# Kernel optimization log

Hardware: AMD Instinct MI355X
Metric: run time of the kernel (lower is better)

The kernel has to match this reference:

```python
import jax, jax.numpy as jnp
import numpy as np

B, P, N, E, H, D = 8, 1000, 1000, 128, 8, 16  # batch, pomo, nodes, embed, heads, qkv_dim
SQRT_E = float(np.sqrt(E))
CLIP = 10.0
INV_SQRT_D = 1.0 / float(np.sqrt(D))


def _heads(x):
    # [b, n, H*D] -> [b, H, n, D]
    b, n, _ = x.shape
    return x.reshape(b, n, H, D).transpose(0, 2, 1, 3)


def _mha(q, k, v, ninf_mask):
    # q: [b,H,P,D], k/v: [b,H,N,D], ninf_mask: [b,P,N]
    score = jnp.einsum('bhnd,bhsd->bhns', q, k) * INV_SQRT_D
    score = score + ninf_mask[:, None, :, :]
    w = jax.nn.softmax(score, axis=-1)
    out = jnp.einsum('bhns,bhsd->bhnd', w, v)
    return out.transpose(0, 2, 1, 3).reshape(q.shape[0], q.shape[2], H * D)


def setup_inputs() -> dict:
    key = jax.random.key(0)
    ks = jax.random.split(key, 16)
    s = 0.02
    return {
        'encoded_last_node': jax.random.normal(ks[0], (B, P, E), jnp.float32),
        'attr': jax.random.normal(ks[1], (B, P, 4), jnp.float32),
        'encoded_nodes': jax.random.normal(ks[2], (B, N, E), jnp.float32),
        'ninf_mask': jnp.zeros((B, P, N), jnp.float32),
        'Wq_shared': jax.random.normal(ks[3], (E + 4, H * D), jnp.float32) * s,
        'Wk_shared': jax.random.normal(ks[4], (E, H * D), jnp.float32) * s,
        'Wv_shared': jax.random.normal(ks[5], (E, H * D), jnp.float32) * s,
        'Wq_task': jax.random.normal(ks[6], (E + 4, H * D), jnp.float32) * s,
        'Wk_task': jax.random.normal(ks[7], (E, H * D), jnp.float32) * s,
        'Wv_task': jax.random.normal(ks[8], (E, H * D), jnp.float32) * s,
        'Wc_shared': jax.random.normal(ks[9], (H * D, E), jnp.float32) * s,
        'bc_shared': jnp.zeros((E,), jnp.float32),
        'Wc_task': jax.random.normal(ks[10], (H * D, E), jnp.float32) * s,
        'bc_task': jnp.zeros((E,), jnp.float32),
        'Wg': jax.random.normal(ks[11], (E + 4, E), jnp.float32) * s,
        'bg': jnp.zeros((E,), jnp.float32),
    }


def reference(encoded_last_node, attr, encoded_nodes, ninf_mask,
              Wq_shared, Wk_shared, Wv_shared, Wq_task, Wk_task, Wv_task,
              Wc_shared, bc_shared, Wc_task, bc_task, Wg, bg):
    # set_kv
    k_shared = _heads(encoded_nodes @ Wk_shared)
    v_shared = _heads(encoded_nodes @ Wv_shared)
    k_task = _heads(encoded_nodes @ Wk_task)
    v_task = _heads(encoded_nodes @ Wv_task)

    # decoder forward
    input_cat = jnp.concatenate([encoded_last_node, attr], axis=2)  # [B,P,E+4]
    q_shared = _heads(input_cat @ Wq_shared)
    q_task = _heads(input_cat @ Wq_task)

    out_shared = _mha(q_shared, k_shared, v_shared, ninf_mask) @ Wc_shared + bc_shared
    out_task = _mha(q_task, k_task, v_task, ninf_mask) @ Wc_task + bc_task

    gate = jax.nn.sigmoid(input_cat @ Wg + bg)
    gated_out = gate * out_shared + (1.0 - gate) * out_task  # [B,P,E]

    # pointer scores against single-head key (encoded_nodes)
    score = jnp.einsum('bpe,bne->bpn', gated_out, encoded_nodes) / SQRT_E
    score_clipped = CLIP * jnp.tanh(score)
    probs = jax.nn.softmax(score_clipped + ninf_mask, axis=2)
    return probs
```

## Files before the change

kernel.cpp:

```cpp
#include <hip/hip_runtime.h>
#include <math.h>

#define BB 8
#define PP 1000
#define NN 1000
#define EE 128
#define HH 8
#define DD 16

#define INV_SQRT_E 0.08838834764831845f
#define INV_SQRT_D 0.25f

typedef short short8_t __attribute__((ext_vector_type(8)));
typedef float f32x4    __attribute__((ext_vector_type(4)));
typedef float f32x16   __attribute__((ext_vector_type(16)));
typedef __bf16 bf16x4  __attribute__((ext_vector_type(4)));
typedef __bf16 bf16x8  __attribute__((ext_vector_type(8)));

__device__ __forceinline__ float sigmoid_fast(float x) {
    return 1.f / (1.f + __expf(-x));
}
__device__ __forceinline__ float tanh_fast(float x) {
    x = fminf(fmaxf(x, -15.f), 15.f);
    float e = __expf(2.f * x);
    return (e - 1.f) / (e + 1.f);
}

__device__ __forceinline__ f32x4 mfma16(short8_t a, short8_t b, f32x4 c) {
    return __builtin_amdgcn_mfma_f32_16x16x32_bf16(a, b, c, 0, 0, 0);
}
__device__ __forceinline__ f32x16 mfma32(short8_t a, short8_t b, f32x16 c) {
    return __builtin_amdgcn_mfma_f32_32x32x16_bf16(a, b, c, 0, 0, 0);
}

__device__ __forceinline__ float sum16(float x) {
    int v;
    v = __builtin_amdgcn_update_dpp(0, __builtin_bit_cast(int, x), 0xB1, 0xF, 0xF, true);
    x += __builtin_bit_cast(float, v);
    v = __builtin_amdgcn_update_dpp(0, __builtin_bit_cast(int, x), 0x4E, 0xF, 0xF, true);
    x += __builtin_bit_cast(float, v);
    v = __builtin_amdgcn_update_dpp(0, __builtin_bit_cast(int, x), 0x141, 0xF, 0xF, true);
    x += __builtin_bit_cast(float, v);
    v = __builtin_amdgcn_update_dpp(0, __builtin_bit_cast(int, x), 0x140, 0xF, 0xF, true);
    x += __builtin_bit_cast(float, v);
    return x;
}

__device__ __forceinline__ unsigned int pack_bf16(float a, float b) {
    __bf16 x = (__bf16)a, y = (__bf16)b;
    unsigned short ux = __builtin_bit_cast(unsigned short, x);
    unsigned short uy = __builtin_bit_cast(unsigned short, y);
    return (unsigned int)ux | ((unsigned int)uy << 16);
}

__global__ __launch_bounds__(256) void conv_w_kernel(
    const float* __restrict__ Wk_s, const float* __restrict__ Wv_s,
    const float* __restrict__ Wk_t, const float* __restrict__ Wv_t,
    const float* __restrict__ Wq_s, const float* __restrict__ Wq_t,
    const float* __restrict__ Wg,   const float* __restrict__ Wc_s,
    const float* __restrict__ Wc_t, __bf16* __restrict__ Wtb)
{
    const int m = blockIdx.x, kt = blockIdx.y;
    const float* srcs[9] = {Wk_s, Wv_s, Wk_t, Wv_t, Wq_s, Wq_t, Wg, Wc_s, Wc_t};
    const int   srcKs[9] = {128, 128, 128, 128, 132, 132, 132, 128, 128};
    const int   kpads[9] = {128, 128, 128, 128, 160, 160, 160, 128, 128};
    const size_t offs[9] = {0, 16384, 32768, 49152, 65536, 86016, 106496, 126976, 143360};
    const int kp = kpads[m];
    if (kt * 32 >= kp) return;
    const float* src = srcs[m];
    const int sK = srcKs[m];
    const size_t off = offs[m];
    __shared__ float tile[32][129];
    const int tid = threadIdx.x;
    for (int j = tid; j < 32 * 128; j += 256) {
        int kk = j >> 7, n = j & 127;
        int k = kt * 32 + kk;
        tile[kk][n] = (k < sK) ? src[(size_t)k * 128 + n] : 0.f;
    }
    __syncthreads();
    for (int j = tid; j < 32 * 128; j += 256) {
        int n = j >> 5, kk = j & 31;
        Wtb[off + (size_t)n * kp + kt * 32 + kk] = (__bf16)tile[kk][n];
    }
}

__global__ __launch_bounds__(256) void to_bf16_kernel(
    const float* __restrict__ in, __bf16* __restrict__ outb)
{
    int i = (blockIdx.x * 256 + threadIdx.x) * 4;
    float4 v = *(const float4*)&in[i];
    bf16x4 pk = { (__bf16)v.x, (__bf16)v.y, (__bf16)v.z, (__bf16)v.w };
    *(bf16x4*)&outb[i] = pk;
}

__global__ __launch_bounds__(256) void concat_inb_kernel(
    const float* __restrict__ eln, const float* __restrict__ attr,
    __bf16* __restrict__ inb)
{
    int t = blockIdx.x * 256 + threadIdx.x;
    int row = t / 20, seg = t - row * 20;
    bf16x8 o = {};
    if (seg < 16) {
        const float* p = &eln[(size_t)row * 128 + seg * 8];
        float4 a = *(const float4*)p, b = *(const float4*)(p + 4);
        o = bf16x8{ (__bf16)a.x, (__bf16)a.y, (__bf16)a.z, (__bf16)a.w,
                    (__bf16)b.x, (__bf16)b.y, (__bf16)b.z, (__bf16)b.w };
    } else if (seg == 16) {
        float4 a = *(const float4*)&attr[(size_t)row * 4];
        o = bf16x8{ (__bf16)a.x, (__bf16)a.y, (__bf16)a.z, (__bf16)a.w,
                    (__bf16)0.f, (__bf16)0.f, (__bf16)0.f, (__bf16)0.f };
    }
    *(bf16x8*)&inb[(size_t)row * 160 + seg * 8] = o;
}

template<int NC>
__device__ __forceinline__ void proj_body(
    const __bf16* __restrict__ A, const __bf16* __restrict__ W,
    f32x4 acc[8], int r0, int quad, int lq)
{
    const int K = NC * 32;
    short8_t aF[NC];
    #pragma unroll
    for (int c = 0; c < NC; ++c)
        aF[c] = *(const short8_t*)&A[(size_t)(r0 + lq) * K + c * 32 + quad * 8];
    #pragma unroll
    for (int nt = 0; nt < 8; ++nt) {
        acc[nt] = f32x4{0.f, 0.f, 0.f, 0.f};
        #pragma unroll
        for (int c = 0; c < NC; ++c) {
            short8_t bF = *(const short8_t*)&W[(size_t)(nt * 16 + lq) * K + c * 32 + quad * 8];
            acc[nt] = mfma16(aF[c], bF, acc[nt]);
        }
    }
}

__global__ __launch_bounds__(256) void proj_mfma_kernel(
    const __bf16* __restrict__ nodesb, const __bf16* __restrict__ inb,
    const __bf16* __restrict__ Wtb, const float* __restrict__ bg,
    __bf16* __restrict__ kb_s, __bf16* __restrict__ vt_s,
    __bf16* __restrict__ kb_t, __bf16* __restrict__ vt_t,
    __bf16* __restrict__ qb_s, __bf16* __restrict__ qb_t,
    float* __restrict__ gate)
{
    const int wsel = blockIdx.y;
    const int wave = threadIdx.x >> 6, lane = threadIdx.x & 63;
    const int quad = lane >> 4, lq = lane & 15;
    const int r0 = blockIdx.x * 64 + wave * 16;

    f32x4 acc[8];
    if (wsel < 4) {
        proj_body<4>(nodesb, Wtb + (size_t)wsel * 16384, acc, r0, quad, lq);
    } else {
        proj_body<5>(inb, Wtb + 65536 + (size_t)(wsel - 4) * 20480, acc, r0, quad, lq);
    }

    if (wsel == 0 || wsel == 2 || wsel == 4 || wsel == 5) {
        __bf16* O = (wsel == 0) ? kb_s : (wsel == 2) ? kb_t : (wsel == 4) ? qb_s : qb_t;
        #pragma unroll
        for (int r = 0; r < 4; ++r) {
            int m = r0 + quad * 4 + r;
            int b = m / 1000, n = m - b * 1000;
            #pragma unroll
            for (int nt = 0; nt < 8; ++nt)
                O[(((size_t)(b * 8 + nt) * 1000 + n) << 4) + lq] = (__bf16)acc[nt][r];
        }
    } else if (wsel == 1 || wsel == 3) {
        __bf16* O = (wsel == 1) ? vt_s : vt_t;
        #pragma unroll
        for (int r = 0; r < 4; ++r) {
            int m = r0 + quad * 4 + r;
            int b = m / 1000, n = m - b * 1000;
            int rr = n & 31;
            int pos = (n & ~31) + ((rr < 16) ? (rr << 1) : (((rr - 16) << 1) | 1));
            #pragma unroll
            for (int nt = 0; nt < 8; ++nt)
                O[(((size_t)(b * 8 + nt) * 16 + lq) << 10) + pos] = (__bf16)acc[nt][r];
        }
    } else {
        #pragma unroll
        for (int nt = 0; nt < 8; ++nt) {
            float bias = bg[nt * 16 + lq];
            #pragma unroll
            for (int r = 0; r < 4; ++r) {
                int m = r0 + quad * 4 + r;
                gate[(size_t)m * 128 + nt * 16 + lq] = sigmoid_fast(acc[nt][r] + bias);
            }
        }
    }
}

__global__ __launch_bounds__(256) void attn_mfma_kernel(
    const __bf16* __restrict__ qb_s, const __bf16* __restrict__ qb_t,
    const __bf16* __restrict__ kb_s, const __bf16* __restrict__ kb_t,
    const __bf16* __restrict__ vt_s, const __bf16* __restrict__ vt_t,
    const float* __restrict__ mask,
    float* __restrict__ att_s, float* __restrict__ att_t)
{
    const int b    = blockIdx.z;
    const int wave = threadIdx.x >> 6;
    const int combo = blockIdx.y * 4 + wave;
    const int br = combo & 1;
    const int h  = combo >> 1;
    const __bf16* Q  = br ? qb_t : qb_s;
    const __bf16* K  = br ? kb_t : kb_s;
    const __bf16* Vt = br ? vt_t : vt_s;
    float* O         = br ? att_t : att_s;
    const int lane = threadIdx.x & 63;
    const int quad = lane >> 4, lq = lane & 15;
    const int col  = lane & 31;
    const int half = lane >> 5;
    const int bh = b * HH + h;
    const int p0 = blockIdx.x * 32;

    __shared__ __align__(16) __bf16 S[4][32][36];

    int pq = p0 + col; if (pq > 999) pq = 999;
    short8_t qA = *(const short8_t*)&Q[(((size_t)bh * 1000 + pq) << 4) + half * 8];

    short8_t onesB = { (short)0x3F80, (short)0x3F80, (short)0x3F80, (short)0x3F80,
                       (short)0x3F80, (short)0x3F80, (short)0x3F80, (short)0x3F80 };

    f32x4 o[2] = { {0.f,0.f,0.f,0.f}, {0.f,0.f,0.f,0.f} };
    f32x4 l[2] = { {0.f,0.f,0.f,0.f}, {0.f,0.f,0.f,0.f} };

    const float* mrow[8];
    #pragma unroll
    for (int j = 0; j < 8; ++j) {
        int row = p0 + ((2 * j) & 3) + 8 * (j >> 1) + 4 * half;
        if (row > 998) row = 998;
        mrow[j] = mask + ((size_t)b * 1000 + row) * 1000 + col;
    }

    short8_t kBc = *(const short8_t*)&K[(((size_t)bh * 1000 + col) << 4) + half * 8];
    short8_t vBc = *(const short8_t*)&Vt[(((size_t)bh * 16 + lq) << 10) + quad * 8];

    for (int n0 = 0; n0 < 992; n0 += 32) {
        int nk = n0 + 32 + col; if (nk > 999) nk = 999;
        short8_t kBn = *(const short8_t*)&K[(((size_t)bh * 1000 + nk) << 4) + half * 8];
        short8_t vBn = *(const short8_t*)&Vt[(((size_t)bh * 16 + lq) << 10) + n0 + 32 + quad * 8];

        float mk[16];
        #pragma unroll
        for (int j = 0; j < 8; ++j) {
            mk[2 * j]     = mrow[j][0];
            mk[2 * j + 1] = mrow[j][1000];
            mrow[j] += 32;
        }

        f32x16 s = mfma32(qA, kBc, f32x16{});

        __threadfence_block();
        #pragma unroll
        for (int reg = 0; reg < 16; ++reg) {
            float e = __expf(fmaf(s[reg], INV_SQRT_D, mk[reg]));
            S[wave][(reg & 3) + 8 * (reg >> 2) + 4 * half][col] = (__bf16)e;
        }
        __threadfence_block();

        #pragma unroll
        for (int t = 0; t < 2; ++t) {
            uint2 L = *(const uint2*)&S[wave][t * 16 + lq][quad * 4];
            uint2 H = *(const uint2*)&S[wave][t * 16 + lq][16 + quad * 4];
            unsigned u0 = __builtin_amdgcn_perm(H.x, L.x, 0x05040100u);
            unsigned u1 = __builtin_amdgcn_perm(H.x, L.x, 0x07060302u);
            unsigned u2 = __builtin_amdgcn_perm(H.y, L.y, 0x05040100u);
            unsigned u3 = __builtin_amdgcn_perm(H.y, L.y, 0x07060302u);
            uint4 u4 = make_uint4(u0, u1, u2, u3);
            short8_t aP = __builtin_bit_cast(short8_t, u4);
            o[t] = mfma16(aP, vBc, o[t]);
            l[t] = mfma16(aP, onesB, l[t]);
        }
        kBc = kBn; vBc = vBn;
    }

    {
        f32x16 s = mfma32(qA, kBc, f32x16{});
        __threadfence_block();
        #pragma unroll
        for (int reg = 0; reg < 16; ++reg) {
            int j = reg >> 1;
            float mkv = (col < 8) ? ((reg & 1) ? mrow[j][1000] : mrow[j][0]) : 0.f;
            float e = (col < 8) ? __expf(fmaf(s[reg], INV_SQRT_D, mkv)) : 0.f;
            S[wave][(reg & 3) + 8 * (reg >> 2) + 4 * half][col] = (__bf16)e;
        }
        __threadfence_block();
        #pragma unroll
        for (int t = 0; t < 2; ++t) {
            uint2 L = *(const uint2*)&S[wave][t * 16 + lq][quad * 4];
            uint2 H = *(const uint2*)&S[wave][t * 16 + lq][16 + quad * 4];
            unsigned u0 = __builtin_amdgcn_perm(H.x, L.x, 0x05040100u);
            unsigned u1 = __builtin_amdgcn_perm(H.x, L.x, 0x07060302u);
            unsigned u2 = __builtin_amdgcn_perm(H.y, L.y, 0x05040100u);
            unsigned u3 = __builtin_amdgcn_perm(H.y, L.y, 0x07060302u);
            uint4 u4 = make_uint4(u0, u1, u2, u3);
            short8_t aP = __builtin_bit_cast(short8_t, u4);
            o[t] = mfma16(aP, vBc, o[t]);
            l[t] = mfma16(aP, onesB, l[t]);
        }
    }

    #pragma unroll
    for (int t = 0; t < 2; ++t)
        #pragma unroll
        for (int r = 0; r < 4; ++r) {
            int p = p0 + t * 16 + quad * 4 + r;
            if (p < 1000)
                O[((size_t)b * 1000 + p) * 128 + h * 16 + lq] = o[t][r] / l[t][r];
        }
}

__global__ __launch_bounds__(256) void combine_mfma_kernel(
    const float* __restrict__ att_s, const float* __restrict__ att_t,
    const __bf16* __restrict__ Wtb,
    const float* __restrict__ bc_s, const float* __restrict__ bc_t,
    const float* __restrict__ gate, __bf16* __restrict__ gatedb)
{
    const int wave = threadIdx.x >> 6, lane = threadIdx.x & 63;
    const int quad = lane >> 4, lq = lane & 15;
    const int r0 = blockIdx.x * 64 + wave * 16;
    const __bf16* Ws = Wtb + 126976;
    const __bf16* Wt = Wtb + 143360;

    short8_t aS[4], aT[4];
    #pragma unroll
    for (int c = 0; c < 4; ++c) {
        const float* ps = &att_s[(size_t)(r0 + lq) * 128 + c * 32 + quad * 8];
        const float* pt = &att_t[(size_t)(r0 + lq) * 128 + c * 32 + quad * 8];
        float4 x = *(const float4*)ps, y = *(const float4*)(ps + 4);
        bf16x8 s8 = { (__bf16)x.x, (__bf16)x.y, (__bf16)x.z, (__bf16)x.w,
                      (__bf16)y.x, (__bf16)y.y, (__bf16)y.z, (__bf16)y.w };
        aS[c] = __builtin_bit_cast(short8_t, s8);
        x = *(const float4*)pt; y = *(const float4*)(pt + 4);
        bf16x8 t8 = { (__bf16)x.x, (__bf16)x.y, (__bf16)x.z, (__bf16)x.w,
                      (__bf16)y.x, (__bf16)y.y, (__bf16)y.z, (__bf16)y.w };
        aT[c] = __builtin_bit_cast(short8_t, t8);
    }
    f32x4 accS[8], accT[8];
    #pragma unroll
    for (int nt = 0; nt < 8; ++nt) {
        accS[nt] = f32x4{0.f,0.f,0.f,0.f};
        accT[nt] = f32x4{0.f,0.f,0.f,0.f};
        #pragma unroll
        for (int c = 0; c < 4; ++c) {
            short8_t bS = *(const short8_t*)&Ws[(size_t)(nt * 16 + lq) * 128 + c * 32 + quad * 8];
            short8_t bT = *(const short8_t*)&Wt[(size_t)(nt * 16 + lq) * 128 + c * 32 + quad * 8];
            accS[nt] = mfma16(aS[c], bS, accS[nt]);
            accT[nt] = mfma16(aT[c], bT, accT[nt]);
        }
    }
    #pragma unroll
    for (int nt = 0; nt < 8; ++nt) {
        int f = nt * 16 + lq;
        float b1 = bc_s[f], b2 = bc_t[f];
        #pragma unroll
        for (int r = 0; r < 4; ++r) {
            int m = r0 + quad * 4 + r;
            float g = gate[(size_t)m * 128 + f];
            float val = g * (accS[nt][r] + b1) + (1.f - g) * (accT[nt][r] + b2);
            gatedb[(size_t)m * 128 + f] = (__bf16)val;
        }
    }
}

__global__ __launch_bounds__(256) void pointer_softmax_kernel(
    const __bf16* __restrict__ gb, const __bf16* __restrict__ nb,
    const float* __restrict__ mask, float* __restrict__ out)
{
    const int b    = blockIdx.y;
    const int p0   = blockIdx.x * 16;
    const int wave = threadIdx.x >> 6;
    const int lane = threadIdx.x & 63;
    const int quad = lane >> 4, lq = lane & 15;

    __shared__ float Spart[4][16];

    short8_t aF[4];
    {
        int pp = p0 + lq; if (pp > 999) pp = 999;
        const __bf16* arow = gb + (((size_t)b * 1000 + pp) << 7) + quad * 8;
        #pragma unroll
        for (int kc = 0; kc < 4; ++kc) aF[kc] = *(const short8_t*)&arow[kc * 32];
    }

    float ev[16][4];
    float psum[4] = {0.f, 0.f, 0.f, 0.f};

    #pragma unroll
    for (int i = 0; i < 16; ++i) {
        const int nt = i * 4 + wave;
        const int nn = nt * 16 + lq;
        const bool nv = nn < 1000;
        int nc = nv ? nn : 999;
        const __bf16* brow = nb + (((size_t)b * 1000 + nc) << 7) + quad * 8;
        f32x4 acc = {0.f, 0.f, 0.f, 0.f};
        #pragma unroll
        for (int kc = 0; kc < 4; ++kc) {
            short8_t bF = *(const short8_t*)&brow[kc * 32];
            acc = mfma16(aF[kc], bF, acc);
        }
        #pragma unroll
        for (int r = 0; r < 4; ++r) {
            int p = p0 + quad * 4 + r;
            bool v = nv && (p < 1000);
            size_t midx = v ? ((size_t)b * 1000 + p) * 1000 + nn : 0;
            float mk = mask[midx];
            float sc = 10.f * tanh_fast(acc[r] * INV_SQRT_E);
            float ee = v ? __expf(sc + mk) : 0.f;
            ev[i][r] = ee;
            psum[r] += ee;
        }
    }

    #pragma unroll
    for (int r = 0; r < 4; ++r) psum[r] = sum16(psum[r]);
    if (lq == 0) {
        #pragma unroll
        for (int r = 0; r < 4; ++r) Spart[wave][quad * 4 + r] = psum[r];
    }
    __syncthreads();
    float inv[4];
    #pragma unroll
    for (int r = 0; r < 4; ++r) {
        int row = quad * 4 + r;
        float s = Spart[0][row] + Spart[1][row] + Spart[2][row] + Spart[3][row];
        inv[r] = 1.f / s;
    }

    #pragma unroll
    for (int i = 0; i < 16; ++i) {
        const int nt = i * 4 + wave;
        const int nn = nt * 16 + lq;
        if (nn < 1000) {
            #pragma unroll
            for (int r = 0; r < 4; ++r) {
                int p = p0 + quad * 4 + r;
                if (p < 1000)
                    out[((size_t)b * 1000 + p) * 1000 + nn] = ev[i][r] * inv[r];
            }
        }
    }
}

extern "C" void kernel_launch(void* const* d_in, const int* in_sizes, int n_in,
                              void* d_out, int out_size, void* d_ws, size_t ws_size,
                              hipStream_t stream)
{
    const float* eln   = (const float*)d_in[0];
    const float* attr  = (const float*)d_in[1];
    const float* nodes = (const float*)d_in[2];
    const float* mask  = (const float*)d_in[3];
    const float* Wq_s  = (const float*)d_in[4];
    const float* Wk_s  = (const float*)d_in[5];
    const float* Wv_s  = (const float*)d_in[6];
    const float* Wq_t  = (const float*)d_in[7];
    const float* Wk_t  = (const float*)d_in[8];
    const float* Wv_t  = (const float*)d_in[9];
    const float* Wc_s  = (const float*)d_in[10];
    const float* bc_s  = (const float*)d_in[11];
    const float* Wc_t  = (const float*)d_in[12];
    const float* bc_t  = (const float*)d_in[13];
    const float* Wg    = (const float*)d_in[14];
    const float* bg    = (const float*)d_in[15];
    float* out = (float*)d_out;

    char* w = (char*)d_ws;
    const size_t KB_SZ = (size_t)8 * 8 * 1000 * 16 * 2;
    const size_t VT_SZ = (size_t)8 * 8 * 16 * 1024 * 2;
    const size_t F_SZ  = (size_t)8000 * 128 * 4;
    const size_t H_SZ  = (size_t)8000 * 128 * 2;
    const size_t IN_SZ = (size_t)8000 * 160 * 2;
    __bf16* kb_s = (__bf16*)w;            w += KB_SZ;
    __bf16* kb_t = (__bf16*)w;            w += KB_SZ;
    __bf16* qb_s = (__bf16*)w;            w += KB_SZ;
    __bf16* qb_t = (__bf16*)w;            w += KB_SZ;
    __bf16* vt_s = (__bf16*)w;            w += VT_SZ;
    __bf16* vt_t = (__bf16*)w;            w += VT_SZ;
    float* gate  = (float*)w;             w += F_SZ;
    float* att_s = (float*)w;             w += F_SZ;
    float* att_t = (float*)w;             w += F_SZ;
    __bf16* gatedb = (__bf16*)w;          w += H_SZ;
    __bf16* nodesb = (__bf16*)w;          w += H_SZ;
    __bf16* inb    = (__bf16*)w;          w += IN_SZ;
    __bf16* Wtb    = (__bf16*)w;          w += 320000;

    hipMemsetAsync(vt_s, 0, 2 * VT_SZ, stream);

    conv_w_kernel<<<dim3(9, 5), 256, 0, stream>>>(
        Wk_s, Wv_s, Wk_t, Wv_t, Wq_s, Wq_t, Wg, Wc_s, Wc_t, Wtb);
    to_bf16_kernel<<<dim3(1000), 256, 0, stream>>>(nodes, nodesb);
    concat_inb_kernel<<<dim3(625), 256, 0, stream>>>(eln, attr, inb);
    proj_mfma_kernel<<<dim3(125, 7), 256, 0, stream>>>(
        nodesb, inb, Wtb, bg, kb_s, vt_s, kb_t, vt_t, qb_s, qb_t, gate);
    attn_mfma_kernel<<<dim3(32, 4, 8), 256, 0, stream>>>(
        qb_s, qb_t, kb_s, kb_t, vt_s, vt_t, mask, att_s, att_t);
    combine_mfma_kernel<<<dim3(125), 256, 0, stream>>>(
        att_s, att_t, Wtb, bc_s, bc_t, gate, gatedb);
    pointer_softmax_kernel<<<dim3(63, 8), 256, 0, stream>>>(
        gatedb, nodesb, mask, out);
}
```

Measured before the change: 242.1 us.

## Precompute bf16 exp(mask), fuse prep kernels, move gate into combine

Merges the weight, nodes and input-concat conversion kernels into one prep kernel. That kernel also precomputes exp(mask) as bf16 once, so the attention and pointer kernels read half the mask bytes and multiply by it instead of adding before exp. The 1/sqrt(D) scale is folded into Q at projection time. The gate projection and sigmoid move into the combine kernel, which avoids a float gate buffer. Attention outputs are now stored as bf16. Costs are an extra 16 MB read/write pass over the mask and bf16 rounding of exp(mask), which fails for masks holding large or -inf values if exp underflows in odd ways.

```diff
diff --git a/kernel.cpp b/kernel.cpp
--- a/kernel.cpp
+++ b/kernel.cpp
@@ -46,71 +46,71 @@
     return x;
 }
 
-__device__ __forceinline__ unsigned int pack_bf16(float a, float b) {
-    __bf16 x = (__bf16)a, y = (__bf16)b;
-    unsigned short ux = __builtin_bit_cast(unsigned short, x);
-    unsigned short uy = __builtin_bit_cast(unsigned short, y);
-    return (unsigned int)ux | ((unsigned int)uy << 16);
-}
-
-__global__ __launch_bounds__(256) void conv_w_kernel(
+__global__ __launch_bounds__(256) void prep_kernel(
+    const float* __restrict__ mask, const float* __restrict__ nodes,
+    const float* __restrict__ eln,  const float* __restrict__ attr,
     const float* __restrict__ Wk_s, const float* __restrict__ Wv_s,
     const float* __restrict__ Wk_t, const float* __restrict__ Wv_t,
     const float* __restrict__ Wq_s, const float* __restrict__ Wq_t,
     const float* __restrict__ Wg,   const float* __restrict__ Wc_s,
-    const float* __restrict__ Wc_t, __bf16* __restrict__ Wtb)
-{
-    const int m = blockIdx.x, kt = blockIdx.y;
-    const float* srcs[9] = {Wk_s, Wv_s, Wk_t, Wv_t, Wq_s, Wq_t, Wg, Wc_s, Wc_t};
-    const int   srcKs[9] = {128, 128, 128, 128, 132, 132, 132, 128, 128};
-    const int   kpads[9] = {128, 128, 128, 128, 160, 160, 160, 128, 128};
-    const size_t offs[9] = {0, 16384, 32768, 49152, 65536, 86016, 106496, 126976, 143360};
-    const int kp = kpads[m];
-    if (kt * 32 >= kp) return;
-    const float* src = srcs[m];
-    const int sK = srcKs[m];
-    const size_t off = offs[m];
+    const float* __restrict__ Wc_t,
+    __bf16* __restrict__ emaskb, __bf16* __restrict__ nodesb,
+    __bf16* __restrict__ inb, __bf16* __restrict__ Wtb)
+{
+    const int bx = blockIdx.x;
     __shared__ float tile[32][129];
-    const int tid = threadIdx.x;
-    for (int j = tid; j < 32 * 128; j += 256) {
-        int kk = j >> 7, n = j & 127;
-        int k = kt * 32 + kk;
-        tile[kk][n] = (k < sK) ? src[(size_t)k * 128 + n] : 0.f;
-    }
-    __syncthreads();
-    for (int j = tid; j < 32 * 128; j += 256) {
-        int n = j >> 5, kk = j & 31;
-        Wtb[off + (size_t)n * kp + kt * 32 + kk] = (__bf16)tile[kk][n];
-    }
-}
-
-__global__ __launch_bounds__(256) void to_bf16_kernel(
-    const float* __restrict__ in, __bf16* __restrict__ outb)
-{
-    int i = (blockIdx.x * 256 + threadIdx.x) * 4;
-    float4 v = *(const float4*)&in[i];
-    bf16x4 pk = { (__bf16)v.x, (__bf16)v.y, (__bf16)v.z, (__bf16)v.w };
-    *(bf16x4*)&outb[i] = pk;
-}
-
-__global__ __launch_bounds__(256) void concat_inb_kernel(
-    const float* __restrict__ eln, const float* __restrict__ attr,
-    __bf16* __restrict__ inb)
-{
-    int t = blockIdx.x * 256 + threadIdx.x;
-    int row = t / 20, seg = t - row * 20;
-    bf16x8 o = {};
-    if (seg < 16) {
-        const float* p = &eln[(size_t)row * 128 + seg * 8];
-        float4 a = *(const float4*)p, b = *(const float4*)(p + 4);
-        o = bf16x8{ (__bf16)a.x, (__bf16)a.y, (__bf16)a.z, (__bf16)a.w,
-                    (__bf16)b.x, (__bf16)b.y, (__bf16)b.z, (__bf16)b.w };
-    } else if (seg == 16) {
-        float4 a = *(const float4*)&attr[(size_t)row * 4];
-        o = bf16x8{ (__bf16)a.x, (__bf16)a.y, (__bf16)a.z, (__bf16)a.w,
-                    (__bf16)0.f, (__bf16)0.f, (__bf16)0.f, (__bf16)0.f };
-    }
-    *(bf16x8*)&inb[(size_t)row * 160 + seg * 8] = o;
+    if (bx < 7813) {
+        int i = (bx * 256 + threadIdx.x) * 4;
+        if (i < 8000000) {
+            float4 v = *(const float4*)&mask[i];
+            bf16x4 pk = { (__bf16)__expf(v.x), (__bf16)__expf(v.y),
+                          (__bf16)__expf(v.z), (__bf16)__expf(v.w) };
+            *(bf16x4*)&emaskb[i] = pk;
+        }
+    } else if (bx < 8813) {
+        int i = ((bx - 7813) * 256 + threadIdx.x) * 4;
+        float4 v = *(const float4*)&nodes[i];
+        bf16x4 pk = { (__bf16)v.x, (__bf16)v.y, (__bf16)v.z, (__bf16)v.w };
+        *(bf16x4*)&nodesb[i] = pk;
+    } else if (bx < 9438) {
+        int t = (bx - 8813) * 256 + threadIdx.x;
+        int row = t / 20, seg = t - row * 20;
+        bf16x8 o = {};
+        if (seg < 16) {
+            const float* p = &eln[(size_t)row * 128 + seg * 8];
+            float4 a = *(const float4*)p, b = *(const float4*)(p + 4);
+            o = bf16x8{ (__bf16)a.x, (__bf16)a.y, (__bf16)a.z, (__bf16)a.w,
+                        (__bf16)b.x, (__bf16)b.y, (__bf16)b.z, (__bf16)b.w };
+        } else if (seg == 16) {
+            float4 a = *(const float4*)&attr[(size_t)row * 4];
+            o = bf16x8{ (__bf16)a.x, (__bf16)a.y, (__bf16)a.z, (__bf16)a.w,
+                        (__bf16)0.f, (__bf16)0.f, (__bf16)0.f, (__bf16)0.f };
+        }
+        *(bf16x8*)&inb[(size_t)row * 160 + seg * 8] = o;
+    } else {
+        int idx = bx - 9438;
+        int m = idx / 5, kt = idx - m * 5;
+        const float* srcs[9] = {Wk_s, Wv_s, Wk_t, Wv_t, Wq_s, Wq_t, Wg, Wc_s, Wc_t};
+        const int   srcKs[9] = {128, 128, 128, 128, 132, 132, 132, 128, 128};
+        const int   kpads[9] = {128, 128, 128, 128, 160, 160, 160, 128, 128};
+        const size_t offs[9] = {0, 16384, 32768, 49152, 65536, 86016, 106496, 126976, 143360};
+        const int kp = kpads[m];
+        if (kt * 32 >= kp) return;
+        const float* src = srcs[m];
+        const int sK = srcKs[m];
+        const size_t off = offs[m];
+        const int tid = threadIdx.x;
+        for (int j = tid; j < 32 * 128; j += 256) {
+            int kk = j >> 7, n = j & 127;
+            int k = kt * 32 + kk;
+            tile[kk][n] = (k < sK) ? src[(size_t)k * 128 + n] : 0.f;
+        }
+        __syncthreads();
+        for (int j = tid; j < 32 * 128; j += 256) {
+            int n = j >> 5, kk = j & 31;
+            Wtb[off + (size_t)n * kp + kt * 32 + kk] = (__bf16)tile[kk][n];
+        }
+    }
 }
 
 template<int NC>
@@ -136,11 +136,10 @@
 
 __global__ __launch_bounds__(256) void proj_mfma_kernel(
     const __bf16* __restrict__ nodesb, const __bf16* __restrict__ inb,
-    const __bf16* __restrict__ Wtb, const float* __restrict__ bg,
+    const __bf16* __restrict__ Wtb,
     __bf16* __restrict__ kb_s, __bf16* __restrict__ vt_s,
     __bf16* __restrict__ kb_t, __bf16* __restrict__ vt_t,
-    __bf16* __restrict__ qb_s, __bf16* __restrict__ qb_t,
-    float* __restrict__ gate)
+    __bf16* __restrict__ qb_s, __bf16* __restrict__ qb_t)
 {
     const int wsel = blockIdx.y;
     const int wave = threadIdx.x >> 6, lane = threadIdx.x & 63;
@@ -154,8 +153,8 @@
         proj_body<5>(inb, Wtb + 65536 + (size_t)(wsel - 4) * 20480, acc, r0, quad, lq);
     }
 
-    if (wsel == 0 || wsel == 2 || wsel == 4 || wsel == 5) {
-        __bf16* O = (wsel == 0) ? kb_s : (wsel == 2) ? kb_t : (wsel == 4) ? qb_s : qb_t;
+    if (wsel == 0 || wsel == 2) {
+        __bf16* O = (wsel == 0) ? kb_s : kb_t;
         #pragma unroll
         for (int r = 0; r < 4; ++r) {
             int m = r0 + quad * 4 + r;
@@ -164,7 +163,18 @@
             for (int nt = 0; nt < 8; ++nt)
                 O[(((size_t)(b * 8 + nt) * 1000 + n) << 4) + lq] = (__bf16)acc[nt][r];
         }
-    } else if (wsel == 1 || wsel == 3) {
+    } else if (wsel == 4 || wsel == 5) {
+        __bf16* O = (wsel == 4) ? qb_s : qb_t;
+        #pragma unroll
+        for (int r = 0; r < 4; ++r) {
+            int m = r0 + quad * 4 + r;
+            int b = m / 1000, n = m - b * 1000;
+            #pragma unroll
+            for (int nt = 0; nt < 8; ++nt)
+                O[(((size_t)(b * 8 + nt) * 1000 + n) << 4) + lq] =
+                    (__bf16)(acc[nt][r] * INV_SQRT_D);
+        }
+    } else {
         __bf16* O = (wsel == 1) ? vt_s : vt_t;
         #pragma unroll
         for (int r = 0; r < 4; ++r) {
@@ -176,16 +186,6 @@
             for (int nt = 0; nt < 8; ++nt)
                 O[(((size_t)(b * 8 + nt) * 16 + lq) << 10) + pos] = (__bf16)acc[nt][r];
         }
-    } else {
-        #pragma unroll
-        for (int nt = 0; nt < 8; ++nt) {
-            float bias = bg[nt * 16 + lq];
-            #pragma unroll
-            for (int r = 0; r < 4; ++r) {
-                int m = r0 + quad * 4 + r;
-                gate[(size_t)m * 128 + nt * 16 + lq] = sigmoid_fast(acc[nt][r] + bias);
-            }
-        }
     }
 }
 
@@ -193,8 +193,8 @@
     const __bf16* __restrict__ qb_s, const __bf16* __restrict__ qb_t,
     const __bf16* __restrict__ kb_s, const __bf16* __restrict__ kb_t,
     const __bf16* __restrict__ vt_s, const __bf16* __restrict__ vt_t,
-    const float* __restrict__ mask,
-    float* __restrict__ att_s, float* __restrict__ att_t)
+    const __bf16* __restrict__ emaskb,
+    __bf16* __restrict__ att_s, __bf16* __restrict__ att_t)
 {
     const int b    = blockIdx.z;
     const int wave = threadIdx.x >> 6;
@@ -204,7 +204,7 @@
     const __bf16* Q  = br ? qb_t : qb_s;
     const __bf16* K  = br ? kb_t : kb_s;
     const __bf16* Vt = br ? vt_t : vt_s;
-    float* O         = br ? att_t : att_s;
+    __bf16* O        = br ? att_t : att_s;
     const int lane = threadIdx.x & 63;
     const int quad = lane >> 4, lq = lane & 15;
     const int col  = lane & 31;
@@ -223,12 +223,12 @@
     f32x4 o[2] = { {0.f,0.f,0.f,0.f}, {0.f,0.f,0.f,0.f} };
     f32x4 l[2] = { {0.f,0.f,0.f,0.f}, {0.f,0.f,0.f,0.f} };
 
-    const float* mrow[8];
+    const __bf16* mrow[8];
     #pragma unroll
     for (int j = 0; j < 8; ++j) {
         int row = p0 + ((2 * j) & 3) + 8 * (j >> 1) + 4 * half;
         if (row > 998) row = 998;
-        mrow[j] = mask + ((size_t)b * 1000 + row) * 1000 + col;
+        mrow[j] = emaskb + ((size_t)b * 1000 + row) * 1000 + col;
     }
 
     short8_t kBc = *(const short8_t*)&K[(((size_t)bh * 1000 + col) << 4) + half * 8];
@@ -242,8 +242,8 @@
         float mk[16];
         #pragma unroll
         for (int j = 0; j < 8; ++j) {
-            mk[2 * j]     = mrow[j][0];
-            mk[2 * j + 1] = mrow[j][1000];
+            mk[2 * j]     = (float)mrow[j][0];
+            mk[2 * j + 1] = (float)mrow[j][1000];
             mrow[j] += 32;
         }
 
@@ -252,7 +252,7 @@
         __threadfence_block();
         #pragma unroll
         for (int reg = 0; reg < 16; ++reg) {
-            float e = __expf(fmaf(s[reg], INV_SQRT_D, mk[reg]));
+            float e = __expf(s[reg]) * mk[reg];
             S[wave][(reg & 3) + 8 * (reg >> 2) + 4 * half][col] = (__bf16)e;
         }
         __threadfence_block();
@@ -279,8 +279,8 @@
         #pragma unroll
         for (int reg = 0; reg < 16; ++reg) {
             int j = reg >> 1;
-            float mkv = (col < 8) ? ((reg & 1) ? mrow[j][1000] : mrow[j][0]) : 0.f;
-            float e = (col < 8) ? __expf(fmaf(s[reg], INV_SQRT_D, mkv)) : 0.f;
+            float mkv = (col < 8) ? (float)((reg & 1) ? mrow[j][1000] : mrow[j][0]) : 0.f;
+            float e = __expf(s[reg]) * mkv;
             S[wave][(reg & 3) + 8 * (reg >> 2) + 4 * half][col] = (__bf16)e;
         }
         __threadfence_block();
@@ -305,58 +305,55 @@
         for (int r = 0; r < 4; ++r) {
             int p = p0 + t * 16 + quad * 4 + r;
             if (p < 1000)
-                O[((size_t)b * 1000 + p) * 128 + h * 16 + lq] = o[t][r] / l[t][r];
-        }
-}
-
-__global__ __launch_bounds__(256) void combine_mfma_kernel(
-    const float* __restrict__ att_s, const float* __restrict__ att_t,
-    const __bf16* __restrict__ Wtb,
+                O[((size_t)b * 1000 + p) * 128 + h * 16 + lq] = (__bf16)(o[t][r] / l[t][r]);
+        }
+}
+
+__global__ __launch_bounds__(128) void combine_mfma_kernel(
+    const __bf16* __restrict__ att_s, const __bf16* __restrict__ att_t,
+    const __bf16* __restrict__ inb, const __bf16* __restrict__ Wtb,
     const float* __restrict__ bc_s, const float* __restrict__ bc_t,
-    const float* __restrict__ gate, __bf16* __restrict__ gatedb)
+    const float* __restrict__ bg, __bf16* __restrict__ gatedb)
 {
     const int wave = threadIdx.x >> 6, lane = threadIdx.x & 63;
     const int quad = lane >> 4, lq = lane & 15;
-    const int r0 = blockIdx.x * 64 + wave * 16;
-    const __bf16* Ws = Wtb + 126976;
-    const __bf16* Wt = Wtb + 143360;
-
-    short8_t aS[4], aT[4];
+    const int r0 = blockIdx.x * 32 + wave * 16;
+    const __bf16* Wgp = Wtb + 106496;
+    const __bf16* Ws  = Wtb + 126976;
+    const __bf16* Wt  = Wtb + 143360;
+
+    short8_t aS[4], aT[4], aG[5];
     #pragma unroll
     for (int c = 0; c < 4; ++c) {
-        const float* ps = &att_s[(size_t)(r0 + lq) * 128 + c * 32 + quad * 8];
-        const float* pt = &att_t[(size_t)(r0 + lq) * 128 + c * 32 + quad * 8];
-        float4 x = *(const float4*)ps, y = *(const float4*)(ps + 4);
-        bf16x8 s8 = { (__bf16)x.x, (__bf16)x.y, (__bf16)x.z, (__bf16)x.w,
-                      (__bf16)y.x, (__bf16)y.y, (__bf16)y.z, (__bf16)y.w };
-        aS[c] = __builtin_bit_cast(short8_t, s8);
-        x = *(const float4*)pt; y = *(const float4*)(pt + 4);
-        bf16x8 t8 = { (__bf16)x.x, (__bf16)x.y, (__bf16)x.z, (__bf16)x.w,
-                      (__bf16)y.x, (__bf16)y.y, (__bf16)y.z, (__bf16)y.w };
-        aT[c] = __builtin_bit_cast(short8_t, t8);
-    }
-    f32x4 accS[8], accT[8];
+        aS[c] = *(const short8_t*)&att_s[(size_t)(r0 + lq) * 128 + c * 32 + quad * 8];
+        aT[c] = *(const short8_t*)&att_t[(size_t)(r0 + lq) * 128 + c * 32 + quad * 8];
+    }
+    #pragma unroll
+    for (int c = 0; c < 5; ++c)
+        aG[c] = *(const short8_t*)&inb[(size_t)(r0 + lq) * 160 + c * 32 + quad * 8];
+
     #pragma unroll
     for (int nt = 0; nt < 8; ++nt) {
-        accS[nt] = f32x4{0.f,0.f,0.f,0.f};
-        accT[nt] = f32x4{0.f,0.f,0.f,0.f};
+        f32x4 accS = {0.f,0.f,0.f,0.f}, accT = accS, accG = accS;
         #pragma unroll
         for (int c = 0; c < 4; ++c) {
             short8_t bS = *(const short8_t*)&Ws[(size_t)(nt * 16 + lq) * 128 + c * 32 + quad * 8];
             short8_t bT = *(const short8_t*)&Wt[(size_t)(nt * 16 + lq) * 128 + c * 32 + quad * 8];
-            accS[nt] = mfma16(aS[c], bS, accS[nt]);
-            accT[nt] = mfma16(aT[c], bT, accT[nt]);
-        }
-    }
-    #pragma unroll
-    for (int nt = 0; nt < 8; ++nt) {
+            accS = mfma16(aS[c], bS, accS);
+            accT = mfma16(aT[c], bT, accT);
+        }
+        #pragma unroll
+        for (int c = 0; c < 5; ++c) {
+            short8_t bG = *(const short8_t*)&Wgp[(size_t)(nt * 16 + lq) * 160 + c * 32 + quad * 8];
+            accG = mfma16(aG[c], bG, accG);
+        }
         int f = nt * 16 + lq;
-        float b1 = bc_s[f], b2 = bc_t[f];
+        float b1 = bc_s[f], b2 = bc_t[f], b3 = bg[f];
         #pragma unroll
         for (int r = 0; r < 4; ++r) {
             int m = r0 + quad * 4 + r;
-            float g = gate[(size_t)m * 128 + f];
-            float val = g * (accS[nt][r] + b1) + (1.f - g) * (accT[nt][r] + b2);
+            float g = sigmoid_fast(accG[r] + b3);
+            float val = g * (accS[r] + b1) + (1.f - g) * (accT[r] + b2);
             gatedb[(size_t)m * 128 + f] = (__bf16)val;
         }
     }
@@ -364,7 +361,7 @@
 
 __global__ __launch_bounds__(256) void pointer_softmax_kernel(
     const __bf16* __restrict__ gb, const __bf16* __restrict__ nb,
-    const float* __restrict__ mask, float* __restrict__ out)
+    const __bf16* __restrict__ emaskb, float* __restrict__ out)
 {
     const int b    = blockIdx.y;
     const int p0   = blockIdx.x * 16;
@@ -403,9 +400,9 @@
             int p = p0 + quad * 4 + r;
             bool v = nv && (p < 1000);
             size_t midx = v ? ((size_t)b * 1000 + p) * 1000 + nn : 0;
-            float mk = mask[midx];
+            float mk = (float)emaskb[midx];
             float sc = 10.f * tanh_fast(acc[r] * INV_SQRT_E);
-            float ee = v ? __expf(sc + mk) : 0.f;
+            float ee = v ? __expf(sc) * mk : 0.f;
             ev[i][r] = ee;
             psum[r] += ee;
         }
@@ -464,37 +461,36 @@
     float* out = (float*)d_out;
 
     char* w = (char*)d_ws;
-    const size_t KB_SZ = (size_t)8 * 8 * 1000 * 16 * 2;
-    const size_t VT_SZ = (size_t)8 * 8 * 16 * 1024 * 2;
-    const size_t F_SZ  = (size_t)8000 * 128 * 4;
+    const size_t KB_SZ = (size_t)64 * 1000 * 16 * 2;
+    const size_t VT_SZ = (size_t)64 * 16 * 1024 * 2;
     const size_t H_SZ  = (size_t)8000 * 128 * 2;
     const size_t IN_SZ = (size_t)8000 * 160 * 2;
-    __bf16* kb_s = (__bf16*)w;            w += KB_SZ;
-    __bf16* kb_t = (__bf16*)w;            w += KB_SZ;
-    __bf16* qb_s = (__bf16*)w;            w += KB_SZ;
-    __bf16* qb_t = (__bf16*)w;            w += KB_SZ;
-    __bf16* vt_s = (__bf16*)w;            w += VT_SZ;
-    __bf16* vt_t = (__bf16*)w;            w += VT_SZ;
-    float* gate  = (float*)w;             w += F_SZ;
-    float* att_s = (float*)w;             w += F_SZ;
-    float* att_t = (float*)w;             w += F_SZ;
+    const size_t EM_SZ = (size_t)8000 * 1000 * 2;
+    __bf16* kb_s  = (__bf16*)w;           w += KB_SZ;
+    __bf16* kb_t  = (__bf16*)w;           w += KB_SZ;
+    __bf16* qb_s  = (__bf16*)w;           w += KB_SZ;
+    __bf16* qb_t  = (__bf16*)w;           w += KB_SZ;
+    __bf16* vt_s  = (__bf16*)w;           w += VT_SZ;
+    __bf16* vt_t  = (__bf16*)w;           w += VT_SZ;
+    __bf16* att_s = (__bf16*)w;           w += H_SZ;
+    __bf16* att_t = (__bf16*)w;           w += H_SZ;
     __bf16* gatedb = (__bf16*)w;          w += H_SZ;
     __bf16* nodesb = (__bf16*)w;          w += H_SZ;
     __bf16* inb    = (__bf16*)w;          w += IN_SZ;
+    __bf16* emaskb = (__bf16*)w;          w += EM_SZ;
     __bf16* Wtb    = (__bf16*)w;          w += 320000;
 
     hipMemsetAsync(vt_s, 0, 2 * VT_SZ, stream);
 
-    conv_w_kernel<<<dim3(9, 5), 256, 0, stream>>>(
-        Wk_s, Wv_s, Wk_t, Wv_t, Wq_s, Wq_t, Wg, Wc_s, Wc_t, Wtb);
-    to_bf16_kernel<<<dim3(1000), 256, 0, stream>>>(nodes, nodesb);
-    concat_inb_kernel<<<dim3(625), 256, 0, stream>>>(eln, attr, inb);
-    proj_mfma_kernel<<<dim3(125, 7), 256, 0, stream>>>(
-        nodesb, inb, Wtb, bg, kb_s, vt_s, kb_t, vt_t, qb_s, qb_t, gate);
+    prep_kernel<<<dim3(9483), 256, 0, stream>>>(
+        mask, nodes, eln, attr, Wk_s, Wv_s, Wk_t, Wv_t, Wq_s, Wq_t, Wg,
+        Wc_s, Wc_t, emaskb, nodesb, inb, Wtb);
+    proj_mfma_kernel<<<dim3(125, 6), 256, 0, stream>>>(
+        nodesb, inb, Wtb, kb_s, vt_s, kb_t, vt_t, qb_s, qb_t);
     attn_mfma_kernel<<<dim3(32, 4, 8), 256, 0, stream>>>(
-        qb_s, qb_t, kb_s, kb_t, vt_s, vt_t, mask, att_s, att_t);
-    combine_mfma_kernel<<<dim3(125), 256, 0, stream>>>(
-        att_s, att_t, Wtb, bc_s, bc_t, gate, gatedb);
+        qb_s, qb_t, kb_s, kb_t, vt_s, vt_t, emaskb, att_s, att_t);
+    combine_mfma_kernel<<<dim3(250), 128, 0, stream>>>(
+        att_s, att_t, inb, Wtb, bc_s, bc_t, bg, gatedb);
     pointer_softmax_kernel<<<dim3(63, 8), 256, 0, stream>>>(
-        gatedb, nodesb, mask, out);
-}
+        gatedb, nodesb, emaskb, out);
+}
```

Measured after the change: 229.2 us. -5.3%, faster.
